# Performance work log

Measured on AMD Instinct MI355X. Metric: run time of the kernel, lower is better.

The kernel has to match this reference:

```python
import jax, jax.numpy as jnp
import numpy as np

N = 50000   # number of nodes
E = 25000   # number of hyperedges
IN = 256
OUT = 256
L = 32      # incidence list width (padded with 0)
NEG = -9e15  # matches torch's -9000000000000000.0 (fits in fp32)


def setup_inputs() -> dict:
    key = jax.random.key(0)
    k1, k2, k3, k4, k5 = jax.random.split(key, 5)
    x = jax.random.normal(k1, (N, IN), dtype=jnp.float32)
    seq = jax.random.randint(k2, (E, L), 0, N)      # node ids per hyperedge
    useq = jax.random.randint(k3, (N, L), 0, E)     # edge ids per node
    stdv = 1.0 / np.sqrt(IN)
    W1 = jax.random.uniform(k4, (IN, OUT), minval=-stdv, maxval=stdv, dtype=jnp.float32)
    W2 = jax.random.uniform(k5, (OUT, OUT), minval=-stdv, maxval=stdv, dtype=jnp.float32)
    return {"x": x, "seq": seq, "useq": useq, "W1": W1, "W2": W2}


def _mask_softmax_weights(idx):
    # softmax over where(idx>0, 1, -9e15): uniform weights over non-padding slots
    logits = jnp.where(idx > 0, 1.0, NEG).astype(jnp.float32)
    return jax.nn.softmax(logits, axis=1)


def reference(x, seq, useq, W1, W2):
    x1 = x @ W1                                   # [N, OUT]
    w = _mask_softmax_weights(seq)                # [E, L]
    edge = jnp.einsum('elc,el->ec', x1[seq], w)   # gather + weighted reduce -> [E, OUT]
    # F.dropout is identity in eval mode
    edge = jax.nn.relu(edge)
    e1 = edge @ W2                                # [E, OUT]
    uw = _mask_softmax_weights(useq)              # [N, L]
    node = jnp.einsum('nlc,nl->nc', e1[useq], uw) # [N, OUT]
    return node
```

## Files before the change

### kernel.cpp

```cpp
#include <hip/hip_runtime.h>

constexpr int N_NODES = 50000;
constexpr int N_EDGES = 25000;
constexpr int C = 256;
constexpr int L = 32;

__device__ ushort W1T_g[C * C];
__device__ ushort W2T_g[C * C];

typedef __attribute__((ext_vector_type(8))) short bf16x8;
typedef __attribute__((ext_vector_type(4))) float f32x4;

__device__ __forceinline__ ushort f2bf(float f) {
    union { float f; unsigned int u; } c; c.f = f;
    unsigned int r = c.u + 0x7FFFu + ((c.u >> 16) & 1u);
    return (ushort)(r >> 16);
}
__device__ __forceinline__ float bflo(unsigned int u) {
    union { unsigned int x; float f; } c; c.x = u << 16; return c.f;
}
__device__ __forceinline__ float bfhi(unsigned int u) {
    union { unsigned int x; float f; } c; c.x = u & 0xFFFF0000u; return c.f;
}
__device__ __forceinline__ void acc_uint4(float* acc, const uint4 v) {
    acc[0] += bflo(v.x); acc[1] += bfhi(v.x);
    acc[2] += bflo(v.y); acc[3] += bfhi(v.y);
    acc[4] += bflo(v.z); acc[5] += bfhi(v.z);
    acc[6] += bflo(v.w); acc[7] += bfhi(v.w);
}

__global__ __launch_bounds__(256) void convert_x_kernel(
    const float* __restrict__ x, ushort* __restrict__ xb)
{
    const size_t i = ((size_t)blockIdx.x * 256 + threadIdx.x) * 4;
    const float4 v = *reinterpret_cast<const float4*>(x + i);
    ushort4 o;
    o.x = f2bf(v.x); o.y = f2bf(v.y); o.z = f2bf(v.z); o.w = f2bf(v.w);
    *reinterpret_cast<ushort4*>(xb + i) = o;
}

__global__ __launch_bounds__(256) void wconv_kernel(
    const float* __restrict__ W1, const float* __restrict__ W2)
{
    const float* W  = blockIdx.z ? W2 : W1;
    ushort* WT      = blockIdx.z ? W2T_g : W1T_g;
    __shared__ float t[64][65];
    const int rr = threadIdx.x >> 6;
    const int cc = threadIdx.x & 63;
    const int br = blockIdx.x * 64;
    const int bc = blockIdx.y * 64;
#pragma unroll
    for (int i = 0; i < 16; ++i) {
        const int row = i * 4 + rr;
        t[row][cc] = W[(size_t)(br + row) * C + bc + cc];
    }
    __syncthreads();
#pragma unroll
    for (int i = 0; i < 16; ++i) {
        const int n = i * 4 + rr;
        WT[(size_t)(bc + n) * C + br + cc] = f2bf(t[cc][n]);
    }
}

__global__ __launch_bounds__(256) void gather_edge_kernel(
    const ushort* __restrict__ src, const int* __restrict__ idx,
    ushort* __restrict__ dst, int nrows)
{
    const int row = blockIdx.x * 8 + (threadIdx.x >> 5);
    const int ln  = threadIdx.x & 31;
    if (row >= nrows) return;

    const int myid = idx[(size_t)row * L + ln];
    const unsigned long long b = __ballot(myid > 0);
    const unsigned int halfmask = (unsigned int)(b >> (threadIdx.x & 32));
    const int cnt = __popc(halfmask);

    float acc[8] = {0.f, 0.f, 0.f, 0.f, 0.f, 0.f, 0.f, 0.f};
#pragma unroll
    for (int lb = 0; lb < L; lb += 8) {
        uint4 v[8];
#pragma unroll
        for (int j = 0; j < 8; ++j) {
            const int id = __shfl(myid, lb + j, 32);
            v[j] = *reinterpret_cast<const uint4*>(
                src + (size_t)id * C + ln * 8);
        }
#pragma unroll
        for (int j = 0; j < 8; ++j) acc_uint4(acc, v[j]);
    }
    const uint4 v0 = *reinterpret_cast<const uint4*>(src + ln * 8);
    float x0[8];
    x0[0] = bflo(v0.x); x0[1] = bfhi(v0.x); x0[2] = bflo(v0.y); x0[3] = bfhi(v0.y);
    x0[4] = bflo(v0.z); x0[5] = bfhi(v0.z); x0[6] = bflo(v0.w); x0[7] = bfhi(v0.w);

    const float corr = (cnt == 0) ? 0.f : (float)(L - cnt);
    const float inv  = (cnt == 0) ? (1.f / (float)L) : (1.f / (float)cnt);

    ushort* d = dst + (size_t)row * C + ln * 8;
    uint4 o;
    o.x = (unsigned)f2bf((acc[0] - corr * x0[0]) * inv) |
          ((unsigned)f2bf((acc[1] - corr * x0[1]) * inv) << 16);
    o.y = (unsigned)f2bf((acc[2] - corr * x0[2]) * inv) |
          ((unsigned)f2bf((acc[3] - corr * x0[3]) * inv) << 16);
    o.z = (unsigned)f2bf((acc[4] - corr * x0[4]) * inv) |
          ((unsigned)f2bf((acc[5] - corr * x0[5]) * inv) << 16);
    o.w = (unsigned)f2bf((acc[6] - corr * x0[6]) * inv) |
          ((unsigned)f2bf((acc[7] - corr * x0[7]) * inv) << 16);
    *reinterpret_cast<uint4*>(d) = o;
}

__global__ __launch_bounds__(256) void gather_node_kernel(
    const ushort* __restrict__ src, const int* __restrict__ idx,
    float* __restrict__ dst, int nrows)
{
    constexpr int CH = 64, NCHUNK = 4;
    constexpr int LPR = CH / 8;
    constexpr int RPB = 256 / LPR;
    const int chunk = blockIdx.x & (NCHUNK - 1);
    const int rb    = (int)(blockIdx.x / NCHUNK) * RPB;
    const int t     = threadIdx.x;

    __shared__ int sidx[RPB][33];
#pragma unroll
    for (int i = 0; i < (RPB * L) / 256; ++i) {
        const int flat = i * 256 + t;
        const int r = flat >> 5, l = flat & 31;
        sidx[r][l] = (rb + r < nrows) ? idx[(size_t)(rb + r) * L + l] : 0;
    }
    __syncthreads();

    const int r   = t / LPR;
    const int ch  = chunk * CH + (t % LPR) * 8;
    const int row = rb + r;
    if (row >= nrows) return;

    float acc[8] = {0.f, 0.f, 0.f, 0.f, 0.f, 0.f, 0.f, 0.f};
    int cnt = 0;
#pragma unroll
    for (int lb = 0; lb < L; lb += 8) {
        uint4 v[8];
#pragma unroll
        for (int j = 0; j < 8; ++j) {
            const int id = sidx[r][lb + j];
            cnt += (id > 0) ? 1 : 0;
            v[j] = *reinterpret_cast<const uint4*>(
                src + (size_t)id * C + ch);
        }
#pragma unroll
        for (int j = 0; j < 8; ++j) acc_uint4(acc, v[j]);
    }
    const uint4 v0 = *reinterpret_cast<const uint4*>(src + ch);
    float x0[8];
    x0[0] = bflo(v0.x); x0[1] = bfhi(v0.x); x0[2] = bflo(v0.y); x0[3] = bfhi(v0.y);
    x0[4] = bflo(v0.z); x0[5] = bfhi(v0.z); x0[6] = bflo(v0.w); x0[7] = bfhi(v0.w);

    const float corr = (cnt == 0) ? 0.f : (float)(L - cnt);
    const float inv  = (cnt == 0) ? (1.f / (float)L) : (1.f / (float)cnt);

    float* d = dst + (size_t)row * C + ch;
    f32x4 o0 = {(acc[0] - corr * x0[0]) * inv, (acc[1] - corr * x0[1]) * inv,
                (acc[2] - corr * x0[2]) * inv, (acc[3] - corr * x0[3]) * inv};
    f32x4 o1 = {(acc[4] - corr * x0[4]) * inv, (acc[5] - corr * x0[5]) * inv,
                (acc[6] - corr * x0[6]) * inv, (acc[7] - corr * x0[7]) * inv};
    __builtin_nontemporal_store(o0, reinterpret_cast<f32x4*>(d));
    __builtin_nontemporal_store(o1, reinterpret_cast<f32x4*>(d) + 1);
}

template <bool RELU>
__global__ __launch_bounds__(256) void gemm_mfma_kernel(
    const ushort* __restrict__ A, int which_w,
    ushort* __restrict__ Cmat, int M)
{
    const ushort* __restrict__ BT = which_w ? W2T_g : W1T_g;
    const int wave  = threadIdx.x >> 6;
    const int lane  = threadIdx.x & 63;
    const int quad  = lane >> 4;
    const int l16   = lane & 15;
    const int base  = (blockIdx.x * 4 + wave) * 32;
    const int nbase = blockIdx.y * 128;

    int m0 = base + l16;      if (m0 > M - 1) m0 = M - 1;
    int m1 = base + 16 + l16; if (m1 > M - 1) m1 = M - 1;

    f32x4 acc[2][8];
    const f32x4 zero = {0.f, 0.f, 0.f, 0.f};
#pragma unroll
    for (int p = 0; p < 2; ++p)
#pragma unroll
        for (int t = 0; t < 8; ++t) acc[p][t] = zero;

    const ushort* a0 = A + (size_t)m0 * C + quad * 8;
    const ushort* a1 = A + (size_t)m1 * C + quad * 8;
    const ushort* br = BT + (size_t)(nbase + l16) * C + quad * 8;

#pragma unroll
    for (int k0 = 0; k0 < C; k0 += 32) {
        const bf16x8 av0 = *reinterpret_cast<const bf16x8*>(a0 + k0);
        const bf16x8 av1 = *reinterpret_cast<const bf16x8*>(a1 + k0);
#pragma unroll
        for (int t = 0; t < 8; ++t) {
            const bf16x8 b = *reinterpret_cast<const bf16x8*>(
                br + (size_t)t * 16 * C + k0);
            acc[0][t] = __builtin_amdgcn_mfma_f32_16x16x32_bf16(av0, b, acc[0][t], 0, 0, 0);
            acc[1][t] = __builtin_amdgcn_mfma_f32_16x16x32_bf16(av1, b, acc[1][t], 0, 0, 0);
        }
    }

#pragma unroll
    for (int p = 0; p < 2; ++p)
#pragma unroll
    for (int t = 0; t < 8; ++t)
#pragma unroll
    for (int r = 0; r < 4; ++r) {
        const int gm = base + p * 16 + quad * 4 + r;
        if (gm < M) {
            float v = acc[p][t][r];
            if (RELU) v = fmaxf(v, 0.f);
            Cmat[(size_t)gm * C + nbase + t * 16 + l16] = f2bf(v);
        }
    }
}

extern "C" void kernel_launch(void* const* d_in, const int* in_sizes, int n_in,
                              void* d_out, int out_size, void* d_ws, size_t ws_size,
                              hipStream_t stream) {
    const float* x    = (const float*)d_in[0];
    const int*   seq  = (const int*)d_in[1];
    const int*   useq = (const int*)d_in[2];
    const float* W1   = (const float*)d_in[3];
    const float* W2   = (const float*)d_in[4];
    float* out = (float*)d_out;

    ushort* xb   = (ushort*)d_ws;
    ushort* tmp1 = xb + (size_t)N_NODES * C;
    ushort* edge = tmp1 + (size_t)N_EDGES * C;

    convert_x_kernel<<<dim3((N_NODES * C) / (256 * 4)), dim3(256), 0, stream>>>(x, xb);
    wconv_kernel<<<dim3(4, 4, 2), dim3(256), 0, stream>>>(W1, W2);

    gather_edge_kernel<<<dim3((N_EDGES + 7) / 8), dim3(256), 0, stream>>>(
        xb, seq, tmp1, N_EDGES);

    const dim3 ggrid((N_EDGES + 127) / 128, 2);
    gemm_mfma_kernel<true><<<ggrid, dim3(256), 0, stream>>>(tmp1, 0, edge, N_EDGES);
    gemm_mfma_kernel<false><<<ggrid, dim3(256), 0, stream>>>(edge, 1, tmp1, N_EDGES);

    const int rblk2 = (N_NODES + 31) / 32;
    gather_node_kernel<<<dim3(4 * rblk2), dim3(256), 0, stream>>>(
        tmp1, useq, out, N_NODES);
}
```

Baseline: 278.6 us.

## Fuse incidence gathers with MFMA GEMMs and apply W2 after node gather

Replaces the separate gather and GEMM kernels with one fused kernel. Each block gathers and averages 32 rows into shared memory as bf16, then multiplies them by the transposed weight with MFMA. The W2 multiply moves after the node-level gather, using linearity. This removes the intermediate tmp buffers, their global round trips and two launches. The cost is about twice the W2 GEMM work (50k rows instead of 25k) and scalar fp32 output stores.

After: 281.0 us. About the same (+0.9%).

```diff
diff --git a/kernel.cpp b/kernel.cpp
--- a/kernel.cpp
+++ b/kernel.cpp
@@ -62,161 +62,113 @@
     }
 }
 
-__global__ __launch_bounds__(256) void gather_edge_kernel(
+constexpr int BR = 32;
+constexpr int APITCH = 264;
+
+template <bool RELU, bool OUT_F32>
+__global__ __launch_bounds__(256) void fused_gather_gemm_kernel(
     const ushort* __restrict__ src, const int* __restrict__ idx,
-    ushort* __restrict__ dst, int nrows)
+    int which_w, ushort* __restrict__ dstb, float* __restrict__ dstf, int M)
 {
-    const int row = blockIdx.x * 8 + (threadIdx.x >> 5);
-    const int ln  = threadIdx.x & 31;
-    if (row >= nrows) return;
+    const ushort* __restrict__ BT = which_w ? W2T_g : W1T_g;
+    const int t  = threadIdx.x;
+    const int rb = blockIdx.x * BR;
 
-    const int myid = idx[(size_t)row * L + ln];
-    const unsigned long long b = __ballot(myid > 0);
-    const unsigned int halfmask = (unsigned int)(b >> (threadIdx.x & 32));
-    const int cnt = __popc(halfmask);
+    __shared__ int    sidx[BR][33];
+    __shared__ ushort A_lds[BR][APITCH];
 
-    float acc[8] = {0.f, 0.f, 0.f, 0.f, 0.f, 0.f, 0.f, 0.f};
 #pragma unroll
-    for (int lb = 0; lb < L; lb += 8) {
-        uint4 v[8];
-#pragma unroll
-        for (int j = 0; j < 8; ++j) {
-            const int id = __shfl(myid, lb + j, 32);
-            v[j] = *reinterpret_cast<const uint4*>(
-                src + (size_t)id * C + ln * 8);
-        }
-#pragma unroll
-        for (int j = 0; j < 8; ++j) acc_uint4(acc, v[j]);
+    for (int i = 0; i < (BR * L) / 256; ++i) {
+        const int flat = i * 256 + t;
+        const int r = flat >> 5, l = flat & 31;
+        sidx[r][l] = (rb + r < M) ? idx[(size_t)(rb + r) * L + l] : 0;
     }
+    __syncthreads();
+
+    const int hw = t >> 5;
+    const int ln = t & 31;
+
     const uint4 v0 = *reinterpret_cast<const uint4*>(src + ln * 8);
     float x0[8];
     x0[0] = bflo(v0.x); x0[1] = bfhi(v0.x); x0[2] = bflo(v0.y); x0[3] = bfhi(v0.y);
     x0[4] = bflo(v0.z); x0[5] = bfhi(v0.z); x0[6] = bflo(v0.w); x0[7] = bfhi(v0.w);
 
-    const float corr = (cnt == 0) ? 0.f : (float)(L - cnt);
-    const float inv  = (cnt == 0) ? (1.f / (float)L) : (1.f / (float)cnt);
-
-    ushort* d = dst + (size_t)row * C + ln * 8;
-    uint4 o;
-    o.x = (unsigned)f2bf((acc[0] - corr * x0[0]) * inv) |
-          ((unsigned)f2bf((acc[1] - corr * x0[1]) * inv) << 16);
-    o.y = (unsigned)f2bf((acc[2] - corr * x0[2]) * inv) |
-          ((unsigned)f2bf((acc[3] - corr * x0[3]) * inv) << 16);
-    o.z = (unsigned)f2bf((acc[4] - corr * x0[4]) * inv) |
-          ((unsigned)f2bf((acc[5] - corr * x0[5]) * inv) << 16);
-    o.w = (unsigned)f2bf((acc[6] - corr * x0[6]) * inv) |
-          ((unsigned)f2bf((acc[7] - corr * x0[7]) * inv) << 16);
-    *reinterpret_cast<uint4*>(d) = o;
-}
-
-__global__ __launch_bounds__(256) void gather_node_kernel(
-    const ushort* __restrict__ src, const int* __restrict__ idx,
-    float* __restrict__ dst, int nrows)
-{
-    constexpr int CH = 64, NCHUNK = 4;
-    constexpr int LPR = CH / 8;
-    constexpr int RPB = 256 / LPR;
-    const int chunk = blockIdx.x & (NCHUNK - 1);
-    const int rb    = (int)(blockIdx.x / NCHUNK) * RPB;
-    const int t     = threadIdx.x;
-
-    __shared__ int sidx[RPB][33];
 #pragma unroll
-    for (int i = 0; i < (RPB * L) / 256; ++i) {
-        const int flat = i * 256 + t;
-        const int r = flat >> 5, l = flat & 31;
-        sidx[r][l] = (rb + r < nrows) ? idx[(size_t)(rb + r) * L + l] : 0;
+    for (int p = 0; p < 4; ++p) {
+        const int r = p * 8 + hw;
+        float acc[8] = {0.f, 0.f, 0.f, 0.f, 0.f, 0.f, 0.f, 0.f};
+        int cnt = 0;
+#pragma unroll
+        for (int lb = 0; lb < L; lb += 8) {
+            uint4 v[8];
+#pragma unroll
+            for (int j = 0; j < 8; ++j) {
+                const int id = sidx[r][lb + j];
+                cnt += (id > 0) ? 1 : 0;
+                v[j] = *reinterpret_cast<const uint4*>(
+                    src + (size_t)id * C + ln * 8);
+            }
+#pragma unroll
+            for (int j = 0; j < 8; ++j) acc_uint4(acc, v[j]);
+        }
+        const float corr = (cnt == 0) ? 0.f : (float)(L - cnt);
+        const float inv  = (cnt == 0) ? (1.f / (float)L) : (1.f / (float)cnt);
+        uint4 o;
+        o.x = (unsigned)f2bf((acc[0] - corr * x0[0]) * inv) |
+              ((unsigned)f2bf((acc[1] - corr * x0[1]) * inv) << 16);
+        o.y = (unsigned)f2bf((acc[2] - corr * x0[2]) * inv) |
+              ((unsigned)f2bf((acc[3] - corr * x0[3]) * inv) << 16);
+        o.z = (unsigned)f2bf((acc[4] - corr * x0[4]) * inv) |
+              ((unsigned)f2bf((acc[5] - corr * x0[5]) * inv) << 16);
+        o.w = (unsigned)f2bf((acc[6] - corr * x0[6]) * inv) |
+              ((unsigned)f2bf((acc[7] - corr * x0[7]) * inv) << 16);
+        *reinterpret_cast<uint4*>(&A_lds[r][ln * 8]) = o;
     }
     __syncthreads();
 
-    const int r   = t / LPR;
-    const int ch  = chunk * CH + (t % LPR) * 8;
-    const int row = rb + r;
-    if (row >= nrows) return;
+    const int wave = t >> 6;
+    const int lane = t & 63;
+    const int quad = lane >> 4;
+    const int l16  = lane & 15;
 
-    float acc[8] = {0.f, 0.f, 0.f, 0.f, 0.f, 0.f, 0.f, 0.f};
-    int cnt = 0;
-#pragma unroll
-    for (int lb = 0; lb < L; lb += 8) {
-        uint4 v[8];
-#pragma unroll
-        for (int j = 0; j < 8; ++j) {
-            const int id = sidx[r][lb + j];
-            cnt += (id > 0) ? 1 : 0;
-            v[j] = *reinterpret_cast<const uint4*>(
-                src + (size_t)id * C + ch);
-        }
-#pragma unroll
-        for (int j = 0; j < 8; ++j) acc_uint4(acc, v[j]);
-    }
-    const uint4 v0 = *reinterpret_cast<const uint4*>(src + ch);
-    float x0[8];
-    x0[0] = bflo(v0.x); x0[1] = bfhi(v0.x); x0[2] = bflo(v0.y); x0[3] = bfhi(v0.y);
-    x0[4] = bflo(v0.z); x0[5] = bfhi(v0.z); x0[6] = bflo(v0.w); x0[7] = bfhi(v0.w);
-
-    const float corr = (cnt == 0) ? 0.f : (float)(L - cnt);
-    const float inv  = (cnt == 0) ? (1.f / (float)L) : (1.f / (float)cnt);
-
-    float* d = dst + (size_t)row * C + ch;
-    f32x4 o0 = {(acc[0] - corr * x0[0]) * inv, (acc[1] - corr * x0[1]) * inv,
-                (acc[2] - corr * x0[2]) * inv, (acc[3] - corr * x0[3]) * inv};
-    f32x4 o1 = {(acc[4] - corr * x0[4]) * inv, (acc[5] - corr * x0[5]) * inv,
-                (acc[6] - corr * x0[6]) * inv, (acc[7] - corr * x0[7]) * inv};
-    __builtin_nontemporal_store(o0, reinterpret_cast<f32x4*>(d));
-    __builtin_nontemporal_store(o1, reinterpret_cast<f32x4*>(d) + 1);
-}
-
-template <bool RELU>
-__global__ __launch_bounds__(256) void gemm_mfma_kernel(
-    const ushort* __restrict__ A, int which_w,
-    ushort* __restrict__ Cmat, int M)
-{
-    const ushort* __restrict__ BT = which_w ? W2T_g : W1T_g;
-    const int wave  = threadIdx.x >> 6;
-    const int lane  = threadIdx.x & 63;
-    const int quad  = lane >> 4;
-    const int l16   = lane & 15;
-    const int base  = (blockIdx.x * 4 + wave) * 32;
-    const int nbase = blockIdx.y * 128;
-
-    int m0 = base + l16;      if (m0 > M - 1) m0 = M - 1;
-    int m1 = base + 16 + l16; if (m1 > M - 1) m1 = M - 1;
-
-    f32x4 acc[2][8];
+    f32x4 acc2[2][4];
     const f32x4 zero = {0.f, 0.f, 0.f, 0.f};
 #pragma unroll
     for (int p = 0; p < 2; ++p)
 #pragma unroll
-        for (int t = 0; t < 8; ++t) acc[p][t] = zero;
+        for (int tt = 0; tt < 4; ++tt) acc2[p][tt] = zero;
 
-    const ushort* a0 = A + (size_t)m0 * C + quad * 8;
-    const ushort* a1 = A + (size_t)m1 * C + quad * 8;
-    const ushort* br = BT + (size_t)(nbase + l16) * C + quad * 8;
+    const ushort* br = BT + (size_t)(wave * 64 + l16) * C + quad * 8;
 
 #pragma unroll
     for (int k0 = 0; k0 < C; k0 += 32) {
-        const bf16x8 av0 = *reinterpret_cast<const bf16x8*>(a0 + k0);
-        const bf16x8 av1 = *reinterpret_cast<const bf16x8*>(a1 + k0);
+        const bf16x8 a0 = *reinterpret_cast<const bf16x8*>(&A_lds[l16][quad * 8 + k0]);
+        const bf16x8 a1 = *reinterpret_cast<const bf16x8*>(&A_lds[16 + l16][quad * 8 + k0]);
 #pragma unroll
-        for (int t = 0; t < 8; ++t) {
+        for (int tt = 0; tt < 4; ++tt) {
             const bf16x8 b = *reinterpret_cast<const bf16x8*>(
-                br + (size_t)t * 16 * C + k0);
-            acc[0][t] = __builtin_amdgcn_mfma_f32_16x16x32_bf16(av0, b, acc[0][t], 0, 0, 0);
-            acc[1][t] = __builtin_amdgcn_mfma_f32_16x16x32_bf16(av1, b, acc[1][t], 0, 0, 0);
+                br + (size_t)tt * 16 * C + k0);
+            acc2[0][tt] = __builtin_amdgcn_mfma_f32_16x16x32_bf16(a0, b, acc2[0][tt], 0, 0, 0);
+            acc2[1][tt] = __builtin_amdgcn_mfma_f32_16x16x32_bf16(a1, b, acc2[1][tt], 0, 0, 0);
         }
     }
 
 #pragma unroll
     for (int p = 0; p < 2; ++p)
 #pragma unroll
-    for (int t = 0; t < 8; ++t)
+    for (int tt = 0; tt < 4; ++tt)
 #pragma unroll
     for (int r = 0; r < 4; ++r) {
-        const int gm = base + p * 16 + quad * 4 + r;
+        const int gm = rb + p * 16 + quad * 4 + r;
         if (gm < M) {
-            float v = acc[p][t][r];
+            float v = acc2[p][tt][r];
             if (RELU) v = fmaxf(v, 0.f);
-            Cmat[(size_t)gm * C + nbase + t * 16 + l16] = f2bf(v);
+            const int col = wave * 64 + tt * 16 + l16;
+            if constexpr (OUT_F32) {
+                __builtin_nontemporal_store(v, dstf + (size_t)gm * C + col);
+            } else {
+                dstb[(size_t)gm * C + col] = f2bf(v);
+            }
         }
     }
 }
@@ -232,20 +184,16 @@
     float* out = (float*)d_out;
 
     ushort* xb   = (ushort*)d_ws;
-    ushort* tmp1 = xb + (size_t)N_NODES * C;
-    ushort* edge = tmp1 + (size_t)N_EDGES * C;
+    ushort* edge = xb + (size_t)N_NODES * C;
 
     convert_x_kernel<<<dim3((N_NODES * C) / (256 * 4)), dim3(256), 0, stream>>>(x, xb);
     wconv_kernel<<<dim3(4, 4, 2), dim3(256), 0, stream>>>(W1, W2);
 
-    gather_edge_kernel<<<dim3((N_EDGES + 7) / 8), dim3(256), 0, stream>>>(
-        xb, seq, tmp1, N_EDGES);
+    fused_gather_gemm_kernel<true, false>
+        <<<dim3((N_EDGES + BR - 1) / BR), dim3(256), 0, stream>>>(
+            xb, seq, 0, edge, nullptr, N_EDGES);
 
-    const dim3 ggrid((N_EDGES + 127) / 128, 2);
-    gemm_mfma_kernel<true><<<ggrid, dim3(256), 0, stream>>>(tmp1, 0, edge, N_EDGES);
-    gemm_mfma_kernel<false><<<ggrid, dim3(256), 0, stream>>>(edge, 1, tmp1, N_EDGES);
-
-    const int rblk2 = (N_NODES + 31) / 32;
-    gather_node_kernel<<<dim3(4 * rblk2), dim3(256), 0, stream>>>(
-        tmp1, useq, out, N_NODES);
+    fused_gather_gemm_kernel<false, true>
+        <<<dim3((N_NODES + BR - 1) / BR), dim3(256), 0, stream>>>(
+            edge, useq, 1, nullptr, out, N_NODES);
 }
```

## Fuse edge gather-mean with first GEMM via LDS-staged A tile

Applied to the files above, without the earlier changes.

Replaces the separate edge gather kernel and first GEMM launch with one kernel. It gathers 32 edge rows into LDS as bf16, then runs MFMA against W1T read from global memory, applying ReLU on output. This removes one launch and the round trip of the intermediate edge tensor through global memory. In exchange each block reloads the whole W1T from global/L2 for only 32 rows, and the B operand is not staged in LDS, which may raise L2 traffic.

Result: faster. 272.8 us (-2.1%).

```diff
diff --git a/kernel.cpp b/kernel.cpp
--- a/kernel.cpp
+++ b/kernel.cpp
@@ -62,51 +62,115 @@
     }
 }
 
-__global__ __launch_bounds__(256) void gather_edge_kernel(
+constexpr int BR = 32;
+constexpr int APITCH = 264;
+
+template <bool RELU, bool OUT_F32>
+__global__ __launch_bounds__(256) void fused_gather_gemm_kernel(
     const ushort* __restrict__ src, const int* __restrict__ idx,
-    ushort* __restrict__ dst, int nrows)
-{
-    const int row = blockIdx.x * 8 + (threadIdx.x >> 5);
-    const int ln  = threadIdx.x & 31;
-    if (row >= nrows) return;
-
-    const int myid = idx[(size_t)row * L + ln];
-    const unsigned long long b = __ballot(myid > 0);
-    const unsigned int halfmask = (unsigned int)(b >> (threadIdx.x & 32));
-    const int cnt = __popc(halfmask);
-
-    float acc[8] = {0.f, 0.f, 0.f, 0.f, 0.f, 0.f, 0.f, 0.f};
-#pragma unroll
-    for (int lb = 0; lb < L; lb += 8) {
-        uint4 v[8];
-#pragma unroll
-        for (int j = 0; j < 8; ++j) {
-            const int id = __shfl(myid, lb + j, 32);
-            v[j] = *reinterpret_cast<const uint4*>(
-                src + (size_t)id * C + ln * 8);
-        }
-#pragma unroll
-        for (int j = 0; j < 8; ++j) acc_uint4(acc, v[j]);
-    }
+    int which_w, ushort* __restrict__ dstb, float* __restrict__ dstf, int M)
+{
+    const ushort* __restrict__ BT = which_w ? W2T_g : W1T_g;
+    const int t  = threadIdx.x;
+    const int rb = blockIdx.x * BR;
+
+    __shared__ int    sidx[BR][33];
+    __shared__ ushort A_lds[BR][APITCH];
+
+#pragma unroll
+    for (int i = 0; i < (BR * L) / 256; ++i) {
+        const int flat = i * 256 + t;
+        const int r = flat >> 5, l = flat & 31;
+        sidx[r][l] = (rb + r < M) ? idx[(size_t)(rb + r) * L + l] : 0;
+    }
+    __syncthreads();
+
+    const int hw = t >> 5;
+    const int ln = t & 31;
+
     const uint4 v0 = *reinterpret_cast<const uint4*>(src + ln * 8);
     float x0[8];
     x0[0] = bflo(v0.x); x0[1] = bfhi(v0.x); x0[2] = bflo(v0.y); x0[3] = bfhi(v0.y);
     x0[4] = bflo(v0.z); x0[5] = bfhi(v0.z); x0[6] = bflo(v0.w); x0[7] = bfhi(v0.w);
 
-    const float corr = (cnt == 0) ? 0.f : (float)(L - cnt);
-    const float inv  = (cnt == 0) ? (1.f / (float)L) : (1.f / (float)cnt);
-
-    ushort* d = dst + (size_t)row * C + ln * 8;
-    uint4 o;
-    o.x = (unsigned)f2bf((acc[0] - corr * x0[0]) * inv) |
-          ((unsigned)f2bf((acc[1] - corr * x0[1]) * inv) << 16);
-    o.y = (unsigned)f2bf((acc[2] - corr * x0[2]) * inv) |
-          ((unsigned)f2bf((acc[3] - corr * x0[3]) * inv) << 16);
-    o.z = (unsigned)f2bf((acc[4] - corr * x0[4]) * inv) |
-          ((unsigned)f2bf((acc[5] - corr * x0[5]) * inv) << 16);
-    o.w = (unsigned)f2bf((acc[6] - corr * x0[6]) * inv) |
-          ((unsigned)f2bf((acc[7] - corr * x0[7]) * inv) << 16);
-    *reinterpret_cast<uint4*>(d) = o;
+#pragma unroll
+    for (int p = 0; p < 4; ++p) {
+        const int r = p * 8 + hw;
+        float acc[8] = {0.f, 0.f, 0.f, 0.f, 0.f, 0.f, 0.f, 0.f};
+        int cnt = 0;
+#pragma unroll
+        for (int lb = 0; lb < L; lb += 8) {
+            uint4 v[8];
+#pragma unroll
+            for (int j = 0; j < 8; ++j) {
+                const int id = sidx[r][lb + j];
+                cnt += (id > 0) ? 1 : 0;
+                v[j] = *reinterpret_cast<const uint4*>(
+                    src + (size_t)id * C + ln * 8);
+            }
+#pragma unroll
+            for (int j = 0; j < 8; ++j) acc_uint4(acc, v[j]);
+        }
+        const float corr = (cnt == 0) ? 0.f : (float)(L - cnt);
+        const float inv  = (cnt == 0) ? (1.f / (float)L) : (1.f / (float)cnt);
+        uint4 o;
+        o.x = (unsigned)f2bf((acc[0] - corr * x0[0]) * inv) |
+              ((unsigned)f2bf((acc[1] - corr * x0[1]) * inv) << 16);
+        o.y = (unsigned)f2bf((acc[2] - corr * x0[2]) * inv) |
+              ((unsigned)f2bf((acc[3] - corr * x0[3]) * inv) << 16);
+        o.z = (unsigned)f2bf((acc[4] - corr * x0[4]) * inv) |
+              ((unsigned)f2bf((acc[5] - corr * x0[5]) * inv) << 16);
+        o.w = (unsigned)f2bf((acc[6] - corr * x0[6]) * inv) |
+              ((unsigned)f2bf((acc[7] - corr * x0[7]) * inv) << 16);
+        *reinterpret_cast<uint4*>(&A_lds[r][ln * 8]) = o;
+    }
+    __syncthreads();
+
+    const int wave = t >> 6;
+    const int lane = t & 63;
+    const int quad = lane >> 4;
+    const int l16  = lane & 15;
+
+    f32x4 acc2[2][4];
+    const f32x4 zero = {0.f, 0.f, 0.f, 0.f};
+#pragma unroll
+    for (int p = 0; p < 2; ++p)
+#pragma unroll
+        for (int tt = 0; tt < 4; ++tt) acc2[p][tt] = zero;
+
+    const ushort* br = BT + (size_t)(wave * 64 + l16) * C + quad * 8;
+
+#pragma unroll
+    for (int k0 = 0; k0 < C; k0 += 32) {
+        const bf16x8 a0 = *reinterpret_cast<const bf16x8*>(&A_lds[l16][quad * 8 + k0]);
+        const bf16x8 a1 = *reinterpret_cast<const bf16x8*>(&A_lds[16 + l16][quad * 8 + k0]);
+#pragma unroll
+        for (int tt = 0; tt < 4; ++tt) {
+            const bf16x8 b = *reinterpret_cast<const bf16x8*>(
+                br + (size_t)tt * 16 * C + k0);
+            acc2[0][tt] = __builtin_amdgcn_mfma_f32_16x16x32_bf16(a0, b, acc2[0][tt], 0, 0, 0);
+            acc2[1][tt] = __builtin_amdgcn_mfma_f32_16x16x32_bf16(a1, b, acc2[1][tt], 0, 0, 0);
+        }
+    }
+
+#pragma unroll
+    for (int p = 0; p < 2; ++p)
+#pragma unroll
+    for (int tt = 0; tt < 4; ++tt)
+#pragma unroll
+    for (int r = 0; r < 4; ++r) {
+        const int gm = rb + p * 16 + quad * 4 + r;
+        if (gm < M) {
+            float v = acc2[p][tt][r];
+            if (RELU) v = fmaxf(v, 0.f);
+            const int col = wave * 64 + tt * 16 + l16;
+            if constexpr (OUT_F32) {
+                __builtin_nontemporal_store(v, dstf + (size_t)gm * C + col);
+            } else {
+                dstb[(size_t)gm * C + col] = f2bf(v);
+            }
+        }
+    }
 }
 
 __global__ __launch_bounds__(256) void gather_node_kernel(
@@ -232,20 +296,20 @@
     float* out = (float*)d_out;
 
     ushort* xb   = (ushort*)d_ws;
-    ushort* tmp1 = xb + (size_t)N_NODES * C;
-    ushort* edge = tmp1 + (size_t)N_EDGES * C;
+    ushort* edge = xb + (size_t)N_NODES * C;
+    ushort* e1   = edge + (size_t)N_EDGES * C;
 
     convert_x_kernel<<<dim3((N_NODES * C) / (256 * 4)), dim3(256), 0, stream>>>(x, xb);
     wconv_kernel<<<dim3(4, 4, 2), dim3(256), 0, stream>>>(W1, W2);
 
-    gather_edge_kernel<<<dim3((N_EDGES + 7) / 8), dim3(256), 0, stream>>>(
-        xb, seq, tmp1, N_EDGES);
-
-    const dim3 ggrid((N_EDGES + 127) / 128, 2);
-    gemm_mfma_kernel<true><<<ggrid, dim3(256), 0, stream>>>(tmp1, 0, edge, N_EDGES);
-    gemm_mfma_kernel<false><<<ggrid, dim3(256), 0, stream>>>(edge, 1, tmp1, N_EDGES);
+    fused_gather_gemm_kernel<true, false>
+        <<<dim3((N_EDGES + BR - 1) / BR), dim3(256), 0, stream>>>(
+            xb, seq, 0, edge, nullptr, N_EDGES);
+
+    gemm_mfma_kernel<false><<<dim3((N_EDGES + 127) / 128, 2), dim3(256), 0, stream>>>(
+        edge, 1, e1, N_EDGES);
 
     const int rblk2 = (N_NODES + 31) / 32;
     gather_node_kernel<<<dim3(4 * rblk2), dim3(256), 0, stream>>>(
-        tmp1, useq, out, N_NODES);
-}
+        e1, useq, out, N_NODES);
+}
```
